# Kernel tuning notes

Hardware: AMD Instinct MI355X
Metric: run time of the kernel (lower is better)

Reference implementation:

```python
import jax, jax.numpy as jnp
import numpy as np

LOG2PI = float(np.log(2.0 * np.pi))
B, D = 8192, 4096


def setup_inputs() -> dict:
    key = jax.random.key(0)
    k1, k2, k3, k4, k5 = jax.random.split(key, 5)
    return {
        "z": jax.random.normal(k1, (B, D), dtype=jnp.float32),
        "mean": jax.random.normal(k2, (B, D), dtype=jnp.float32),
        "log_sd": jax.random.normal(k3, (B, D), dtype=jnp.float32),
        "target": jax.random.randint(k4, (B,), 0, 2, dtype=jnp.int64 if jax.config.jax_enable_x64 else jnp.int32),
        "logdet": jax.random.normal(k5, (B,), dtype=jnp.float32),
    }


def reference(z, mean, log_sd, target, logdet):
    # Per-class (binary) masked statistics, exactly matching the torch forward:
    #   mu_cls = mean[target==j].mean(0); log_sd_cls likewise;
    #   log_p  = gaussian_log_p(z_cls, mu_cls, log_sd_cls).sum(feature).mean(batch)
    def per_class(j):
        m = (target == j).astype(z.dtype)          # (B,)
        cnt = m.sum()
        ld_mean = (logdet * m).sum() / cnt          # scalar
        mu = (mean * m[:, None]).sum(0) / cnt       # (D,)
        lsd = (log_sd * m[:, None]).sum(0) / cnt    # (D,)
        # gaussian log-prob summed over features, per sample -> (B,)
        lp = (-0.5 * LOG2PI - lsd
              - 0.5 * (z - mu) ** 2 * jnp.exp(-2.0 * lsd)).sum(1)
        lp_mean = (lp * m).sum() / cnt              # masked mean over class members
        return ld_mean, mu, lsd, lp_mean

    res = [per_class(j) for j in (0, 1)]
    logdet_total = jnp.stack([r[0] for r in res])   # (2,)
    mus_per_class = jnp.stack([r[1] for r in res])  # (2, D)
    log_sds_per_class = jnp.stack([r[2] for r in res])  # (2, D)
    log_p_total = jnp.stack([r[3] for r in res])    # (2,)
    prior_logprob = (log_p_total + logdet_total).mean()
    return prior_logprob, mus_per_class, log_sds_per_class, log_p_total
```

## Files before the change

kernel.cpp:

```cpp
#include <hip/hip_runtime.h>

#define B_SZ 8192
#define D_SZ 4096

constexpr int OFF_SCALAR = 8 * D_SZ;
constexpr int OFF_DBL    = 8 * D_SZ + 8;
constexpr size_t WS_CLEAR_BYTES = (size_t)(8 * D_SZ + 8) * 4 + 4 * 8;

__global__ __launch_bounds__(256)
void count_logdet_kernel(const int* __restrict__ target,
                         const float* __restrict__ logdet,
                         float* __restrict__ ws) {
    float c = 0.f, a = 0.f, o = 0.f;
    for (int i = blockIdx.x * 256 + threadIdx.x; i < B_SZ; i += gridDim.x * 256) {
        const float m  = (target[i] == 1) ? 1.f : 0.f;
        const float ld = logdet[i];
        c += m; a += ld; o += ld * m;
    }
    for (int off = 32; off > 0; off >>= 1) {
        c += __shfl_down(c, off);
        a += __shfl_down(a, off);
        o += __shfl_down(o, off);
    }
    if ((threadIdx.x & 63) == 0) {
        atomicAdd(ws + OFF_SCALAR + 0, c);
        atomicAdd(ws + OFF_SCALAR + 1, a);
        atomicAdd(ws + OFF_SCALAR + 2, o);
    }
}

__global__ __launch_bounds__(256)
void colsum_kernel(const float* __restrict__ z,
                   const float* __restrict__ mean,
                   const float* __restrict__ lsd,
                   const int* __restrict__ target,
                   float* __restrict__ ws) {
    const int col = blockIdx.x * 512 + threadIdx.x * 2;
    const int rows_per = B_SZ / gridDim.y;
    const int r0 = blockIdx.y * rows_per;

    float am0 = 0, am1 = 0, sm0 = 0, sm1 = 0;
    float al0 = 0, al1 = 0, sl0 = 0, sl1 = 0;
    float az0 = 0, az1 = 0, sz0 = 0, sz1 = 0;
    float aq0 = 0, aq1 = 0, sq0 = 0, sq1 = 0;

#pragma unroll 4
    for (int i = r0; i < r0 + rows_per; ++i) {
        const size_t base = (size_t)i * D_SZ + col;
        const float2 vm = *(const float2*)(mean + base);
        const float2 vl = *(const float2*)(lsd + base);
        const float2 vz = *(const float2*)(z + base);
        const float  mk = (target[i] == 1) ? 1.f : 0.f;

        am0 += vm.x;                    am1 += vm.y;
        sm0  = fmaf(vm.x, mk, sm0);     sm1  = fmaf(vm.y, mk, sm1);
        al0 += vl.x;                    al1 += vl.y;
        sl0  = fmaf(vl.x, mk, sl0);     sl1  = fmaf(vl.y, mk, sl1);
        az0 += vz.x;                    az1 += vz.y;
        sz0  = fmaf(vz.x, mk, sz0);     sz1  = fmaf(vz.y, mk, sz1);
        const float q0 = vz.x * vz.x,   q1 = vz.y * vz.y;
        aq0 += q0;                      aq1 += q1;
        sq0  = fmaf(q0, mk, sq0);       sq1  = fmaf(q1, mk, sq1);
    }

    atomicAdd(ws + 0 * D_SZ + col, am0); atomicAdd(ws + 0 * D_SZ + col + 1, am1);
    atomicAdd(ws + 1 * D_SZ + col, sm0); atomicAdd(ws + 1 * D_SZ + col + 1, sm1);
    atomicAdd(ws + 2 * D_SZ + col, al0); atomicAdd(ws + 2 * D_SZ + col + 1, al1);
    atomicAdd(ws + 3 * D_SZ + col, sl0); atomicAdd(ws + 3 * D_SZ + col + 1, sl1);
    atomicAdd(ws + 4 * D_SZ + col, az0); atomicAdd(ws + 4 * D_SZ + col + 1, az1);
    atomicAdd(ws + 5 * D_SZ + col, sz0); atomicAdd(ws + 5 * D_SZ + col + 1, sz1);
    atomicAdd(ws + 6 * D_SZ + col, aq0); atomicAdd(ws + 6 * D_SZ + col + 1, aq1);
    atomicAdd(ws + 7 * D_SZ + col, sq0); atomicAdd(ws + 7 * D_SZ + col + 1, sq1);
}

__global__ __launch_bounds__(256)
void finalize_cols_kernel(float* __restrict__ ws, float* __restrict__ out) {
    const int d = blockIdx.x * 256 + threadIdx.x;
    const float cnt1 = ws[OFF_SCALAR];
    const float cnt0 = (float)B_SZ - cnt1;

    const float ma = ws[0 * D_SZ + d], m1 = ws[1 * D_SZ + d];
    const float la = ws[2 * D_SZ + d], l1 = ws[3 * D_SZ + d];
    const float za = ws[4 * D_SZ + d], z1 = ws[5 * D_SZ + d];
    const float qa = ws[6 * D_SZ + d], q1 = ws[7 * D_SZ + d];

    const float mu1 = m1 / cnt1, mu0 = (ma - m1) / cnt0;
    const float ls1 = l1 / cnt1, ls0 = (la - l1) / cnt0;

    out[1 + d]             = mu0;
    out[1 + D_SZ + d]      = mu1;
    out[1 + 2 * D_SZ + d]  = ls0;
    out[1 + 3 * D_SZ + d]  = ls1;

    const float z0 = za - z1, q0 = qa - q1;
    const double w0 = 0.5 * exp(-2.0 * (double)ls0);
    const double w1 = 0.5 * exp(-2.0 * (double)ls1);
    double S0 = w0 * ((double)q0 - 2.0 * (double)mu0 * (double)z0 + (double)cnt0 * (double)mu0 * (double)mu0);
    double S1 = w1 * ((double)q1 - 2.0 * (double)mu1 * (double)z1 + (double)cnt1 * (double)mu1 * (double)mu1);
    double L0 = (double)ls0;
    double L1 = (double)ls1;

    for (int off = 32; off > 0; off >>= 1) {
        S0 += __shfl_down(S0, off);
        S1 += __shfl_down(S1, off);
        L0 += __shfl_down(L0, off);
        L1 += __shfl_down(L1, off);
    }
    if ((threadIdx.x & 63) == 0) {
        double* wd = (double*)(ws + OFF_DBL);
        atomicAdd(wd + 0, S0);
        atomicAdd(wd + 1, S1);
        atomicAdd(wd + 2, L0);
        atomicAdd(wd + 3, L1);
    }
}

__global__ void finalize_scalars_kernel(const float* __restrict__ ws, float* __restrict__ out) {
    const double LOG2PI = 1.8378770664093453;
    const double* wd = (const double*)(ws + OFF_DBL);
    const double S0 = wd[0], S1 = wd[1], L0 = wd[2], L1 = wd[3];
    const double cnt1 = (double)ws[OFF_SCALAR];
    const double cnt0 = (double)B_SZ - cnt1;
    const double ld_all = (double)ws[OFF_SCALAR + 1];
    const double ld1s   = (double)ws[OFF_SCALAR + 2];

    const double ldm1 = ld1s / cnt1;
    const double ldm0 = (ld_all - ld1s) / cnt0;

    const double c0 = -0.5 * LOG2PI * (double)D_SZ - L0;
    const double c1 = -0.5 * LOG2PI * (double)D_SZ - L1;
    const double lp0 = c0 - S0 / cnt0;
    const double lp1 = c1 - S1 / cnt1;

    out[1 + 4 * D_SZ + 0] = (float)lp0;
    out[1 + 4 * D_SZ + 1] = (float)lp1;
    out[0] = (float)(0.5 * ((lp0 + ldm0) + (lp1 + ldm1)));
}

extern "C" void kernel_launch(void* const* d_in, const int* in_sizes, int n_in,
                              void* d_out, int out_size, void* d_ws, size_t ws_size,
                              hipStream_t stream) {
    const float* z      = (const float*)d_in[0];
    const float* mean   = (const float*)d_in[1];
    const float* log_sd = (const float*)d_in[2];
    const int*   target = (const int*)d_in[3];
    const float* logdet = (const float*)d_in[4];
    float* out = (float*)d_out;
    float* ws  = (float*)d_ws;

    hipMemsetAsync(d_ws, 0, WS_CLEAR_BYTES, stream);

    count_logdet_kernel<<<16, 256, 0, stream>>>(target, logdet, ws);

    dim3 grid(D_SZ / 512, 64);
    colsum_kernel<<<grid, 256, 0, stream>>>(z, mean, log_sd, target, ws);

    finalize_cols_kernel<<<D_SZ / 256, 256, 0, stream>>>(ws, out);
    finalize_scalars_kernel<<<1, 1, 0, stream>>>(ws, out);
}
```

Measured before the change: 95.36 us.

## Split column sums per input tensor, write partials, and reduce without atomics

The column-sum kernel now splits work over a third grid dimension, one slice per input tensor (mean, log_sd, z). It also uses float4 loads and writes per-row-chunk partial sums to workspace instead of doing float atomics. A new reduce kernel sums the R partial slabs, and R is chosen to fit the workspace size. The goal is more parallelism, wider loads and fewer atomic conflicts. The cost is extra partial-sum traffic (up to 16MB written and read again) and one more kernel launch.

New measurement: 109.2 us. +14.5%, slower.

```diff
diff --git a/kernel.cpp b/kernel.cpp
--- a/kernel.cpp
+++ b/kernel.cpp
@@ -3,14 +3,11 @@
 #define B_SZ 8192
 #define D_SZ 4096
 
-constexpr int OFF_SCALAR = 8 * D_SZ;
-constexpr int OFF_DBL    = 8 * D_SZ + 8;
-constexpr size_t WS_CLEAR_BYTES = (size_t)(8 * D_SZ + 8) * 4 + 4 * 8;
 
 __global__ __launch_bounds__(256)
 void count_logdet_kernel(const int* __restrict__ target,
                          const float* __restrict__ logdet,
-                         float* __restrict__ ws) {
+                         float* __restrict__ ws, int sc_off) {
     float c = 0.f, a = 0.f, o = 0.f;
     for (int i = blockIdx.x * 256 + threadIdx.x; i < B_SZ; i += gridDim.x * 256) {
         const float m  = (target[i] == 1) ? 1.f : 0.f;
@@ -23,66 +20,81 @@
         o += __shfl_down(o, off);
     }
     if ((threadIdx.x & 63) == 0) {
-        atomicAdd(ws + OFF_SCALAR + 0, c);
-        atomicAdd(ws + OFF_SCALAR + 1, a);
-        atomicAdd(ws + OFF_SCALAR + 2, o);
+        atomicAdd(ws + sc_off + 0, c);
+        atomicAdd(ws + sc_off + 1, a);
+        atomicAdd(ws + sc_off + 2, o);
     }
 }
 
-__global__ __launch_bounds__(256)
+template <int ROWS_PER>
+__global__ __launch_bounds__(256, 8)
 void colsum_kernel(const float* __restrict__ z,
                    const float* __restrict__ mean,
                    const float* __restrict__ lsd,
                    const int* __restrict__ target,
                    float* __restrict__ ws) {
-    const int col = blockIdx.x * 512 + threadIdx.x * 2;
-    const int rows_per = B_SZ / gridDim.y;
-    const int r0 = blockIdx.y * rows_per;
+    const int col = blockIdx.x * 1024 + threadIdx.x * 4;
+    const int i0  = blockIdx.y * ROWS_PER;
+    float* pbase  = ws + (size_t)blockIdx.y * 8 * D_SZ;
 
-    float am0 = 0, am1 = 0, sm0 = 0, sm1 = 0;
-    float al0 = 0, al1 = 0, sl0 = 0, sl1 = 0;
-    float az0 = 0, az1 = 0, sz0 = 0, sz1 = 0;
-    float aq0 = 0, aq1 = 0, sq0 = 0, sq1 = 0;
-
-#pragma unroll 4
-    for (int i = r0; i < r0 + rows_per; ++i) {
-        const size_t base = (size_t)i * D_SZ + col;
-        const float2 vm = *(const float2*)(mean + base);
-        const float2 vl = *(const float2*)(lsd + base);
-        const float2 vz = *(const float2*)(z + base);
-        const float  mk = (target[i] == 1) ? 1.f : 0.f;
-
-        am0 += vm.x;                    am1 += vm.y;
-        sm0  = fmaf(vm.x, mk, sm0);     sm1  = fmaf(vm.y, mk, sm1);
-        al0 += vl.x;                    al1 += vl.y;
-        sl0  = fmaf(vl.x, mk, sl0);     sl1  = fmaf(vl.y, mk, sl1);
-        az0 += vz.x;                    az1 += vz.y;
-        sz0  = fmaf(vz.x, mk, sz0);     sz1  = fmaf(vz.y, mk, sz1);
-        const float q0 = vz.x * vz.x,   q1 = vz.y * vz.y;
-        aq0 += q0;                      aq1 += q1;
-        sq0  = fmaf(q0, mk, sq0);       sq1  = fmaf(q1, mk, sq1);
+    if (blockIdx.z == 2) {
+        float4 aA = {0,0,0,0}, a1 = {0,0,0,0};
+        float4 qA = {0,0,0,0}, q1 = {0,0,0,0};
+#pragma unroll 8
+        for (int i = i0; i < i0 + ROWS_PER; ++i) {
+            const float4 v = *(const float4*)(z + (size_t)i * D_SZ + col);
+            const float mk = (target[i] == 1) ? 1.f : 0.f;
+            aA.x += v.x; aA.y += v.y; aA.z += v.z; aA.w += v.w;
+            a1.x = fmaf(v.x, mk, a1.x); a1.y = fmaf(v.y, mk, a1.y);
+            a1.z = fmaf(v.z, mk, a1.z); a1.w = fmaf(v.w, mk, a1.w);
+            const float qx = v.x*v.x, qy = v.y*v.y, qz = v.z*v.z, qw = v.w*v.w;
+            qA.x += qx; qA.y += qy; qA.z += qz; qA.w += qw;
+            q1.x = fmaf(qx, mk, q1.x); q1.y = fmaf(qy, mk, q1.y);
+            q1.z = fmaf(qz, mk, q1.z); q1.w = fmaf(qw, mk, q1.w);
+        }
+        *(float4*)(pbase + 4 * D_SZ + col) = aA;
+        *(float4*)(pbase + 5 * D_SZ + col) = a1;
+        *(float4*)(pbase + 6 * D_SZ + col) = qA;
+        *(float4*)(pbase + 7 * D_SZ + col) = q1;
+    } else {
+        const float* p = (blockIdx.z == 0) ? mean : lsd;
+        const int segbase = blockIdx.z * 2;
+        float4 aA = {0,0,0,0}, a1 = {0,0,0,0};
+#pragma unroll 8
+        for (int i = i0; i < i0 + ROWS_PER; ++i) {
+            const float4 v = *(const float4*)(p + (size_t)i * D_SZ + col);
+            const float mk = (target[i] == 1) ? 1.f : 0.f;
+            aA.x += v.x; aA.y += v.y; aA.z += v.z; aA.w += v.w;
+            a1.x = fmaf(v.x, mk, a1.x); a1.y = fmaf(v.y, mk, a1.y);
+            a1.z = fmaf(v.z, mk, a1.z); a1.w = fmaf(v.w, mk, a1.w);
+        }
+        *(float4*)(pbase + (segbase + 0) * D_SZ + col) = aA;
+        *(float4*)(pbase + (segbase + 1) * D_SZ + col) = a1;
     }
-
-    atomicAdd(ws + 0 * D_SZ + col, am0); atomicAdd(ws + 0 * D_SZ + col + 1, am1);
-    atomicAdd(ws + 1 * D_SZ + col, sm0); atomicAdd(ws + 1 * D_SZ + col + 1, sm1);
-    atomicAdd(ws + 2 * D_SZ + col, al0); atomicAdd(ws + 2 * D_SZ + col + 1, al1);
-    atomicAdd(ws + 3 * D_SZ + col, sl0); atomicAdd(ws + 3 * D_SZ + col + 1, sl1);
-    atomicAdd(ws + 4 * D_SZ + col, az0); atomicAdd(ws + 4 * D_SZ + col + 1, az1);
-    atomicAdd(ws + 5 * D_SZ + col, sz0); atomicAdd(ws + 5 * D_SZ + col + 1, sz1);
-    atomicAdd(ws + 6 * D_SZ + col, aq0); atomicAdd(ws + 6 * D_SZ + col + 1, aq1);
-    atomicAdd(ws + 7 * D_SZ + col, sq0); atomicAdd(ws + 7 * D_SZ + col + 1, sq1);
 }
 
 __global__ __launch_bounds__(256)
-void finalize_cols_kernel(float* __restrict__ ws, float* __restrict__ out) {
+void reduce_partials_kernel(const float* __restrict__ ws,
+                            float* __restrict__ red, int R) {
+    const int s = blockIdx.x * 256 + threadIdx.x;
+    float acc = 0.f;
+#pragma unroll 8
+    for (int r = 0; r < R; ++r) acc += ws[(size_t)r * 8 * D_SZ + s];
+    red[s] = acc;
+}
+
+__global__ __launch_bounds__(256)
+void finalize_cols_kernel(const float* __restrict__ red,
+                          float* __restrict__ ws, int sc_off,
+                          float* __restrict__ out) {
     const int d = blockIdx.x * 256 + threadIdx.x;
-    const float cnt1 = ws[OFF_SCALAR];
+    const float cnt1 = ws[sc_off];
     const float cnt0 = (float)B_SZ - cnt1;
 
-    const float ma = ws[0 * D_SZ + d], m1 = ws[1 * D_SZ + d];
-    const float la = ws[2 * D_SZ + d], l1 = ws[3 * D_SZ + d];
-    const float za = ws[4 * D_SZ + d], z1 = ws[5 * D_SZ + d];
-    const float qa = ws[6 * D_SZ + d], q1 = ws[7 * D_SZ + d];
+    const float ma = red[0 * D_SZ + d], m1 = red[1 * D_SZ + d];
+    const float la = red[2 * D_SZ + d], l1 = red[3 * D_SZ + d];
+    const float za = red[4 * D_SZ + d], z1 = red[5 * D_SZ + d];
+    const float qa = red[6 * D_SZ + d], q1 = red[7 * D_SZ + d];
 
     const float mu1 = m1 / cnt1, mu0 = (ma - m1) / cnt0;
     const float ls1 = l1 / cnt1, ls0 = (la - l1) / cnt0;
@@ -107,7 +119,7 @@
         L1 += __shfl_down(L1, off);
     }
     if ((threadIdx.x & 63) == 0) {
-        double* wd = (double*)(ws + OFF_DBL);
+        double* wd = (double*)(ws + sc_off + 8);
         atomicAdd(wd + 0, S0);
         atomicAdd(wd + 1, S1);
         atomicAdd(wd + 2, L0);
@@ -115,14 +127,15 @@
     }
 }
 
-__global__ void finalize_scalars_kernel(const float* __restrict__ ws, float* __restrict__ out) {
+__global__ void finalize_scalars_kernel(const float* __restrict__ ws, int sc_off,
+                                        float* __restrict__ out) {
     const double LOG2PI = 1.8378770664093453;
-    const double* wd = (const double*)(ws + OFF_DBL);
+    const double* wd = (const double*)(ws + sc_off + 8);
     const double S0 = wd[0], S1 = wd[1], L0 = wd[2], L1 = wd[3];
-    const double cnt1 = (double)ws[OFF_SCALAR];
+    const double cnt1 = (double)ws[sc_off];
     const double cnt0 = (double)B_SZ - cnt1;
-    const double ld_all = (double)ws[OFF_SCALAR + 1];
-    const double ld1s   = (double)ws[OFF_SCALAR + 2];
+    const double ld_all = (double)ws[sc_off + 1];
+    const double ld1s   = (double)ws[sc_off + 2];
 
     const double ldm1 = ld1s / cnt1;
     const double ldm0 = (ld_all - ld1s) / cnt0;
@@ -148,13 +161,29 @@
     float* out = (float*)d_out;
     float* ws  = (float*)d_ws;
 
-    hipMemsetAsync(d_ws, 0, WS_CLEAR_BYTES, stream);
+    int R = 128;
+    while (R > 8) {
+        const size_t need = ((size_t)R * 8 * D_SZ + 8 * D_SZ + 8) * 4 + 32;
+        if (need <= ws_size) break;
+        R >>= 1;
+    }
+    const int red_off = R * 8 * D_SZ;
+    const int sc_off  = red_off + 8 * D_SZ;
 
-    count_logdet_kernel<<<16, 256, 0, stream>>>(target, logdet, ws);
+    hipMemsetAsync((char*)d_ws + (size_t)sc_off * 4, 0, 8 * 4 + 4 * 8, stream);
 
-    dim3 grid(D_SZ / 512, 64);
-    colsum_kernel<<<grid, 256, 0, stream>>>(z, mean, log_sd, target, ws);
+    count_logdet_kernel<<<16, 256, 0, stream>>>(target, logdet, ws, sc_off);
 
-    finalize_cols_kernel<<<D_SZ / 256, 256, 0, stream>>>(ws, out);
-    finalize_scalars_kernel<<<1, 1, 0, stream>>>(ws, out);
+    const dim3 grid(D_SZ / 1024, R, 3);
+    switch (R) {
+        case 128: colsum_kernel<B_SZ/128><<<grid, 256, 0, stream>>>(z, mean, log_sd, target, ws); break;
+        case  64: colsum_kernel<B_SZ/64 ><<<grid, 256, 0, stream>>>(z, mean, log_sd, target, ws); break;
+        case  32: colsum_kernel<B_SZ/32 ><<<grid, 256, 0, stream>>>(z, mean, log_sd, target, ws); break;
+        case  16: colsum_kernel<B_SZ/16 ><<<grid, 256, 0, stream>>>(z, mean, log_sd, target, ws); break;
+        default:  colsum_kernel<B_SZ/8  ><<<grid, 256, 0, stream>>>(z, mean, log_sd, target, ws); break;
+    }
+
+    reduce_partials_kernel<<<8 * D_SZ / 256, 256, 0, stream>>>(ws, ws + red_off, R);
+    finalize_cols_kernel<<<D_SZ / 256, 256, 0, stream>>>(ws + red_off, ws, sc_off, out);
+    finalize_scalars_kernel<<<1, 1, 0, stream>>>(ws, sc_off, out);
 }
```
